# Optimization experiments

Measured on AMD Instinct MI355X. Metric: run time of the kernel, lower is better.

The kernel has to match this reference:

```python
import jax, jax.numpy as jnp
import numpy as np

P_ORDER = 3  # cubic B-spline (spline_order in the torch module)


def _make_knots(degree, lo, hi, order):
    # mirrors Transformation.__init__ knot construction
    d = (hi - lo) / (degree - 1)
    return np.linspace(lo - order * d, hi + order * d, degree + 2 * order).astype(np.float32)


def setup_inputs() -> dict:
    key = jax.random.key(0)
    N, V, degree = 500000, 8, 40
    M = degree + P_ORDER - 1  # 42 coefficients per variable
    k1, k2 = jax.random.split(key)
    # data inside the spline range [-3, 3]
    x = jax.random.uniform(k1, (N, V), minval=-2.9, maxval=2.9, dtype=jnp.float32)
    # unrestricted params in the style of compute_starting_values (inverse softplus of increments)
    base = np.linspace(-3.0, 3.0, M).astype(np.float32)
    raw = base.copy()
    raw[1:] = np.log(np.exp(base[1:] - base[:-1]) - 1.0)
    raw_params = jnp.asarray(np.tile(raw[:, None], (1, V)))
    raw_params = raw_params + 0.01 * jax.random.normal(k2, raw_params.shape, dtype=jnp.float32)
    knots = jnp.asarray(np.stack([_make_knots(degree, -3.0, 3.0, P_ORDER) for _ in range(V)], axis=1))  # [46, V]
    return {"x": x, "raw_params": raw_params, "knots": knots}


def _deboor(x, t, c, p):
    # vectorized deBoor evaluation: x [N], knots t [K], coeffs c [K-p-1]
    K = t.shape[0]
    k = jnp.clip(jnp.searchsorted(t, x, side='right') - 1, p, K - p - 2)  # knot span per point
    j = jnp.arange(p + 1)
    d = c[k[:, None] - p + j]  # [N, p+1] local coefficients (gather)
    for r in range(1, p + 1):
        for jj in range(p, r - 1, -1):
            tl = t[jj + k - p]
            tr = t[jj + 1 + k - r]
            alpha = (x - tl) / (tr - tl)
            d = d.at[:, jj].set((1.0 - alpha) * d[:, jj - 1] + alpha * d[:, jj])
    return d[:, p]


def _eval_var(xv, tv, cv):
    p = P_ORDER
    M = cv.shape[0]
    y = _deboor(xv, tv, cv, p)
    # derivative spline: degree p-1, coeffs from first differences of c
    q = p * (cv[1:] - cv[:-1]) / (tv[p + 1:p + M] - tv[1:M])
    dy = _deboor(xv, tv[1:-1], q, p - 1)
    return y, dy


def reference(x, raw_params, knots):
    # restrict_parameters with monotonically_increasing: softplus increments + cumsum
    incr = jnp.concatenate([raw_params[:1], jax.nn.softplus(raw_params[1:])], axis=0)
    c = jnp.cumsum(incr, axis=0)  # [M, V] monotone coefficients
    y, dy = jax.vmap(_eval_var, in_axes=(1, 1, 1), out_axes=1)(x, knots, c)
    log_d = jnp.log(dy)  # log-determinant contribution of the monotone transform
    return y, log_d
```

## Files before the change

### kernel.cpp

```cpp
#include <hip/hip_runtime.h>
#include <cmath>

#define NV    8
#define NM    42
#define NK    46
#define TOT_C (NM * NV)
#define LDS_STRIDE 48

typedef float f32x4 __attribute__((ext_vector_type(4)));

__global__ void prep_kernel(const float* __restrict__ raw,
                            const float* __restrict__ knots,
                            float* __restrict__ c,
                            float* __restrict__ q) {
    __shared__ float s[TOT_C];
    int tid = threadIdx.x;
    if (tid < TOT_C) {
        float r = raw[tid];
        float inc;
        if (tid < NV) {
            inc = r;
        } else {
            inc = (r > 0.f) ? (r + log1pf(expf(-r))) : log1pf(expf(r));
        }
        s[tid] = inc;
    }
    __syncthreads();
    for (int off = 1; off < NM; off <<= 1) {
        float val = 0.f;
        if (tid < TOT_C) {
            int j = tid >> 3;
            val = s[tid] + ((j >= off) ? s[tid - off * NV] : 0.f);
        }
        __syncthreads();
        if (tid < TOT_C) s[tid] = val;
        __syncthreads();
    }
    if (tid < TOT_C) {
        int j = tid >> 3, v = tid & 7;
        float cj = s[tid];
        c[tid] = cj;
        float qj = 0.f;
        if (j < NM - 1) {
            float cn = s[tid + NV];
            qj = 3.f * (cn - cj) / (knots[(j + 4) * NV + v] - knots[(j + 1) * NV + v]);
        }
        q[tid] = qj;
    }
}

__device__ __forceinline__ void eval_one(float xv, int v,
                                         const float* __restrict__ sc,
                                         const float* __restrict__ sq,
                                         const float* __restrict__ st0,
                                         const float* __restrict__ sinvd,
                                         float& yv, float& ldv) {
    float f = (xv - st0[v]) * sinvd[v];
    int k = (int)floorf(f);
    k = min(max(k, 3), NK - 5);
    float u = f - (float)k;
    int base = v * LDS_STRIDE + (k - 3);
    float c0 = sc[base], c1 = sc[base + 1], c2 = sc[base + 2], c3 = sc[base + 3];
    float q0 = sq[base], q1 = sq[base + 1], q2 = sq[base + 2];

    float omu = 1.f - u;
    float u2 = u * u,  o2 = omu * omu;
    float u3 = u2 * u, o3 = o2 * omu;
    const float k6 = 0.16666666666f;
    float B0 = o3 * k6;
    float B3 = u3 * k6;
    float B1 = (3.f * u3 - 6.f * u2 + 4.f) * k6;
    float B2 = 1.f - B0 - B1 - B3;
    yv = fmaf(B0, c0, fmaf(B1, c1, fmaf(B2, c2, B3 * c3)));

    float w0 = 0.5f * o2, w2 = 0.5f * u2, w1 = 1.f - w0 - w2;
    ldv = __logf(fmaf(w0, q0, fmaf(w1, q1, w2 * q2)));
}

__global__ __launch_bounds__(256) void eval_kernel(
        const float* __restrict__ x,
        const float* __restrict__ knots,
        const float* __restrict__ c,
        const float* __restrict__ q,
        float* __restrict__ y_out,
        float* __restrict__ ld_out,
        int total) {
    __shared__ float sc[NV * LDS_STRIDE];
    __shared__ float sq[NV * LDS_STRIDE];
    __shared__ float st0[NV];
    __shared__ float sinvd[NV];
    int tid = threadIdx.x;
    for (int idx = tid; idx < TOT_C; idx += 256) {
        int j = idx >> 3, v = idx & 7;
        sc[v * LDS_STRIDE + j] = c[idx];
        sq[v * LDS_STRIDE + j] = q[idx];
    }
    if (tid < NV) {
        float t0 = knots[tid];
        st0[tid] = t0;
        sinvd[tid] = 1.0f / (knots[NV + tid] - t0);
    }
    __syncthreads();

    int t = blockIdx.x * 256 + tid;
    int i0 = t * 4;
    if (i0 + 3 < total) {
        f32x4 xv = *(const f32x4*)(x + i0);
        int v0 = i0 & (NV - 1);
        float y0, y1, y2, y3, l0, l1, l2, l3;
        eval_one(xv.x, v0,     sc, sq, st0, sinvd, y0, l0);
        eval_one(xv.y, v0 + 1, sc, sq, st0, sinvd, y1, l1);
        eval_one(xv.z, v0 + 2, sc, sq, st0, sinvd, y2, l2);
        eval_one(xv.w, v0 + 3, sc, sq, st0, sinvd, y3, l3);
        f32x4 yv = {y0, y1, y2, y3};
        f32x4 lv = {l0, l1, l2, l3};
        __builtin_nontemporal_store(yv, (f32x4*)(y_out + i0));
        __builtin_nontemporal_store(lv, (f32x4*)(ld_out + i0));
    } else {
        for (int i = i0; i < total; ++i) {
            float yv, lv;
            eval_one(x[i], i & (NV - 1), sc, sq, st0, sinvd, yv, lv);
            y_out[i]  = yv;
            ld_out[i] = lv;
        }
    }
}

extern "C" void kernel_launch(void* const* d_in, const int* in_sizes, int n_in,
                              void* d_out, int out_size, void* d_ws, size_t ws_size,
                              hipStream_t stream) {
    const float* x     = (const float*)d_in[0];
    const float* raw   = (const float*)d_in[1];
    const float* knots = (const float*)d_in[2];

    float* c = (float*)d_ws;
    float* q = c + TOT_C;

    int total = in_sizes[0];
    float* y_out  = (float*)d_out;
    float* ld_out = y_out + total;

    prep_kernel<<<1, 384, 0, stream>>>(raw, knots, c, q);
    int nthreads = (total + 3) / 4;
    int blocks = (nthreads + 255) / 256;
    eval_kernel<<<blocks, 256, 0, stream>>>(x, knots, c, q, y_out, ld_out, total);
}
```

Measured before the change: 81.24 us.

## Fuse coefficient prep into eval kernel with per-span packed LDS records

Removes the separate single-block prep kernel. Every block now recomputes the softplus, cumsum scan and derivative coefficients itself, then packs the 4 spline and 3 derivative coefficients for each knot span into an 8-float LDS record, so each evaluation needs two vector LDS reads. Each thread now handles 8 elements, one full row of variables, so the variable index is a compile-time constant and knot scales sit in registers. In exchange every block repeats the prep work and its barriers, and block size rises to 512.

```diff
diff --git a/kernel.cpp b/kernel.cpp
--- a/kernel.cpp
+++ b/kernel.cpp
@@ -5,123 +5,132 @@
 #define NM    42
 #define NK    46
 #define TOT_C (NM * NV)
-#define LDS_STRIDE 48
+#define NRK   39
+#define NRECS (NV * NRK)
+#define REC_F 8
+#define TPB   512
+#define EPT   8
 
 typedef float f32x4 __attribute__((ext_vector_type(4)));
 
-__global__ void prep_kernel(const float* __restrict__ raw,
-                            const float* __restrict__ knots,
-                            float* __restrict__ c,
-                            float* __restrict__ q) {
+__global__ __launch_bounds__(TPB) void fused_kernel(
+        const float* __restrict__ x,
+        const float* __restrict__ raw,
+        const float* __restrict__ knots,
+        float* __restrict__ y_out,
+        float* __restrict__ ld_out,
+        int total)
+{
     __shared__ float s[TOT_C];
+    __shared__ __align__(32) float rec[NRECS * REC_F];
+
     int tid = threadIdx.x;
+
     if (tid < TOT_C) {
         float r = raw[tid];
-        float inc;
-        if (tid < NV) {
-            inc = r;
-        } else {
-            inc = (r > 0.f) ? (r + log1pf(expf(-r))) : log1pf(expf(r));
-        }
+        float inc = (tid < NV) ? r
+                  : ((r > 0.f) ? (r + log1pf(expf(-r))) : log1pf(expf(r)));
         s[tid] = inc;
     }
     __syncthreads();
+
     for (int off = 1; off < NM; off <<= 1) {
-        float val = 0.f;
+        float a = 0.f;
         if (tid < TOT_C) {
             int j = tid >> 3;
-            val = s[tid] + ((j >= off) ? s[tid - off * NV] : 0.f);
+            a = s[tid] + ((j >= off) ? s[tid - off * NV] : 0.f);
         }
         __syncthreads();
-        if (tid < TOT_C) s[tid] = val;
+        if (tid < TOT_C) s[tid] = a;
         __syncthreads();
     }
-    if (tid < TOT_C) {
-        int j = tid >> 3, v = tid & 7;
-        float cj = s[tid];
-        c[tid] = cj;
-        float qj = 0.f;
-        if (j < NM - 1) {
-            float cn = s[tid + NV];
-            qj = 3.f * (cn - cj) / (knots[(j + 4) * NV + v] - knots[(j + 1) * NV + v]);
-        }
-        q[tid] = qj;
-    }
-}
 
-__device__ __forceinline__ void eval_one(float xv, int v,
-                                         const float* __restrict__ sc,
-                                         const float* __restrict__ sq,
-                                         const float* __restrict__ st0,
-                                         const float* __restrict__ sinvd,
-                                         float& yv, float& ldv) {
-    float f = (xv - st0[v]) * sinvd[v];
-    int k = (int)floorf(f);
-    k = min(max(k, 3), NK - 5);
-    float u = f - (float)k;
-    int base = v * LDS_STRIDE + (k - 3);
-    float c0 = sc[base], c1 = sc[base + 1], c2 = sc[base + 2], c3 = sc[base + 3];
-    float q0 = sq[base], q1 = sq[base + 1], q2 = sq[base + 2];
-
-    float omu = 1.f - u;
-    float u2 = u * u,  o2 = omu * omu;
-    float u3 = u2 * u, o3 = o2 * omu;
-    const float k6 = 0.16666666666f;
-    float B0 = o3 * k6;
-    float B3 = u3 * k6;
-    float B1 = (3.f * u3 - 6.f * u2 + 4.f) * k6;
-    float B2 = 1.f - B0 - B1 - B3;
-    yv = fmaf(B0, c0, fmaf(B1, c1, fmaf(B2, c2, B3 * c3)));
-
-    float w0 = 0.5f * o2, w2 = 0.5f * u2, w1 = 1.f - w0 - w2;
-    ldv = __logf(fmaf(w0, q0, fmaf(w1, q1, w2 * q2)));
-}
-
-__global__ __launch_bounds__(256) void eval_kernel(
-        const float* __restrict__ x,
-        const float* __restrict__ knots,
-        const float* __restrict__ c,
-        const float* __restrict__ q,
-        float* __restrict__ y_out,
-        float* __restrict__ ld_out,
-        int total) {
-    __shared__ float sc[NV * LDS_STRIDE];
-    __shared__ float sq[NV * LDS_STRIDE];
-    __shared__ float st0[NV];
-    __shared__ float sinvd[NV];
-    int tid = threadIdx.x;
-    for (int idx = tid; idx < TOT_C; idx += 256) {
-        int j = idx >> 3, v = idx & 7;
-        sc[v * LDS_STRIDE + j] = c[idx];
-        sq[v * LDS_STRIDE + j] = q[idx];
-    }
-    if (tid < NV) {
-        float t0 = knots[tid];
-        st0[tid] = t0;
-        sinvd[tid] = 1.0f / (knots[NV + tid] - t0);
+    if (tid < NRECS) {
+        int v  = tid / NRK;
+        int kk = tid - v * NRK;
+        float c0 = s[(kk + 0) * NV + v];
+        float c1 = s[(kk + 1) * NV + v];
+        float c2 = s[(kk + 2) * NV + v];
+        float c3 = s[(kk + 3) * NV + v];
+        float q0 = 3.f * (c1 - c0) / (knots[(kk + 4) * NV + v] - knots[(kk + 1) * NV + v]);
+        float q1 = 3.f * (c2 - c1) / (knots[(kk + 5) * NV + v] - knots[(kk + 2) * NV + v]);
+        float q2 = 3.f * (c3 - c2) / (knots[(kk + 6) * NV + v] - knots[(kk + 3) * NV + v]);
+        f32x4 lo = {c0, c1, c2, c3};
+        f32x4 hi = {q0, q1, q2, 0.f};
+        f32x4* rp = (f32x4*)&rec[tid * REC_F];
+        rp[0] = lo;
+        rp[1] = hi;
     }
     __syncthreads();
 
-    int t = blockIdx.x * 256 + tid;
-    int i0 = t * 4;
-    if (i0 + 3 < total) {
-        f32x4 xv = *(const f32x4*)(x + i0);
-        int v0 = i0 & (NV - 1);
-        float y0, y1, y2, y3, l0, l1, l2, l3;
-        eval_one(xv.x, v0,     sc, sq, st0, sinvd, y0, l0);
-        eval_one(xv.y, v0 + 1, sc, sq, st0, sinvd, y1, l1);
-        eval_one(xv.z, v0 + 2, sc, sq, st0, sinvd, y2, l2);
-        eval_one(xv.w, v0 + 3, sc, sq, st0, sinvd, y3, l3);
-        f32x4 yv = {y0, y1, y2, y3};
-        f32x4 lv = {l0, l1, l2, l3};
-        __builtin_nontemporal_store(yv, (f32x4*)(y_out + i0));
-        __builtin_nontemporal_store(lv, (f32x4*)(ld_out + i0));
+    float t0v[NV], invdv[NV];
+    #pragma unroll
+    for (int v = 0; v < NV; ++v) {
+        float t0 = knots[v];
+        t0v[v]   = t0;
+        invdv[v] = 1.f / (knots[NV + v] - t0);
+    }
+
+    const float k6 = 0.16666666666f;
+    int i0 = (blockIdx.x * TPB + tid) * EPT;
+
+    if (i0 + EPT - 1 < total) {
+        f32x4 xa = *(const f32x4*)(x + i0);
+        f32x4 xb = *(const f32x4*)(x + i0 + 4);
+        f32x4 ya, yb, la, lb;
+        #pragma unroll
+        for (int e = 0; e < EPT; ++e) {
+            float xe = (e < 4) ? xa[e] : xb[e - 4];
+            const int v = e;
+            float f = (xe - t0v[v]) * invdv[v];
+            int k = (int)floorf(f);
+            k = min(max(k, 3), NK - 5);
+            float u = f - (float)k;
+            const f32x4* rp = (const f32x4*)&rec[(v * NRK + (k - 3)) * REC_F];
+            f32x4 cc = rp[0];
+            f32x4 qq = rp[1];
+
+            float omu = 1.f - u;
+            float u2 = u * u,  o2 = omu * omu;
+            float u3 = u2 * u, o3 = o2 * omu;
+            float B0 = o3 * k6;
+            float B3 = u3 * k6;
+            float B1 = (3.f * u3 - 6.f * u2 + 4.f) * k6;
+            float B2 = 1.f - B0 - B1 - B3;
+            float yv = fmaf(B0, cc.x, fmaf(B1, cc.y, fmaf(B2, cc.z, B3 * cc.w)));
+
+            float w0 = 0.5f * o2, w2 = 0.5f * u2, w1 = 1.f - w0 - w2;
+            float lv = __logf(fmaf(w0, qq.x, fmaf(w1, qq.y, w2 * qq.z)));
+
+            if (e < 4) { ya[e] = yv; la[e] = lv; }
+            else       { yb[e - 4] = yv; lb[e - 4] = lv; }
+        }
+        __builtin_nontemporal_store(ya, (f32x4*)(y_out + i0));
+        __builtin_nontemporal_store(yb, (f32x4*)(y_out + i0 + 4));
+        __builtin_nontemporal_store(la, (f32x4*)(ld_out + i0));
+        __builtin_nontemporal_store(lb, (f32x4*)(ld_out + i0 + 4));
     } else {
         for (int i = i0; i < total; ++i) {
-            float yv, lv;
-            eval_one(x[i], i & (NV - 1), sc, sq, st0, sinvd, yv, lv);
-            y_out[i]  = yv;
-            ld_out[i] = lv;
+            int v = i & (NV - 1);
+            float t0 = knots[v];
+            float invd = 1.f / (knots[NV + v] - t0);
+            float f = (x[i] - t0) * invd;
+            int k = (int)floorf(f);
+            k = min(max(k, 3), NK - 5);
+            float u = f - (float)k;
+            const float* rp = &rec[(v * NRK + (k - 3)) * REC_F];
+            float c0 = rp[0], c1 = rp[1], c2 = rp[2], c3 = rp[3];
+            float q0 = rp[4], q1 = rp[5], q2 = rp[6];
+            float omu = 1.f - u;
+            float u2 = u * u,  o2 = omu * omu;
+            float u3 = u2 * u, o3 = o2 * omu;
+            float B0 = o3 * k6;
+            float B3 = u3 * k6;
+            float B1 = (3.f * u3 - 6.f * u2 + 4.f) * k6;
+            float B2 = 1.f - B0 - B1 - B3;
+            y_out[i] = fmaf(B0, c0, fmaf(B1, c1, fmaf(B2, c2, B3 * c3)));
+            float w0 = 0.5f * o2, w2 = 0.5f * u2, w1 = 1.f - w0 - w2;
+            ld_out[i] = __logf(fmaf(w0, q0, fmaf(w1, q1, w2 * q2)));
         }
     }
 }
@@ -133,15 +142,11 @@
     const float* raw   = (const float*)d_in[1];
     const float* knots = (const float*)d_in[2];
 
-    float* c = (float*)d_ws;
-    float* q = c + TOT_C;
-
     int total = in_sizes[0];
     float* y_out  = (float*)d_out;
     float* ld_out = y_out + total;
 
-    prep_kernel<<<1, 384, 0, stream>>>(raw, knots, c, q);
-    int nthreads = (total + 3) / 4;
-    int blocks = (nthreads + 255) / 256;
-    eval_kernel<<<blocks, 256, 0, stream>>>(x, knots, c, q, y_out, ld_out, total);
+    int threads_needed = (total + EPT - 1) / EPT;
+    int blocks = (threads_needed + TPB - 1) / TPB;
+    fused_kernel<<<blocks, TPB, 0, stream>>>(x, raw, knots, y_out, ld_out, total);
 }
```

Result: no change. 81.32 us (+0.1%).
